# Kernel optimization log

Measured on AMD Instinct MI355X. Metric: run time of the kernel, lower is better.

Reference implementation:

```python
import jax, jax.numpy as jnp
import numpy as np

B, L, DM = 4, 2048, 1024  # batch, seq len (== l_max, global kernel), d_model; head_dim = 1


def setup_inputs() -> dict:
    key = jax.random.key(0)
    ks = jax.random.split(key, 13)
    n = lambda k, shape, s=1.0: jax.random.normal(k, shape, dtype=jnp.float32) * s
    W_SCALE = 0.02   # keeps activations well-conditioned through the chained convs
    K_SCALE = 0.02
    return {
        "u": n(ks[0], (B, L, DM)),
        "Wq": n(ks[1], (DM, DM), W_SCALE), "bq": n(ks[2], (DM,), W_SCALE),
        "Wk": n(ks[3], (DM, DM), W_SCALE), "bk": n(ks[4], (DM,), W_SCALE),
        "Wv": n(ks[5], (DM, DM), W_SCALE), "bv": n(ks[6], (DM,), W_SCALE),
        "k_kernel": n(ks[7], (DM, L), K_SCALE),
        "k_D": n(ks[8], (DM,)),
        "ssm_kernel": n(ks[9], (DM, L), K_SCALE),
        "D": n(ks[10], (DM,)),
        "Wo": n(ks[11], (DM, DM), W_SCALE), "bo": n(ks[12], (DM,), W_SCALE),
    }


def reference(u, Wq, bq, Wk, bk, Wv, bv, k_kernel, k_D, ssm_kernel, D, Wo, bo):
    # u: (B, L, H) with H = d_model (head_dim = 1)
    Lseq = u.shape[1]
    fft_size = 2 * Lseq  # zero-pad to 2L for linear (causal) convolution

    # q/k/v projections -> (B, H, L)
    q = jnp.einsum('blh,dh->bdl', u, Wq) + bq[None, :, None]
    k = jnp.einsum('blh,dh->bdl', u, Wk) + bk[None, :, None]
    v = jnp.einsum('blh,dh->bdl', u, Wv) + bv[None, :, None]

    # shift conv on k: k <- k_kernel * k (causal FFT conv) + k_D * k
    k_kernel_f = jnp.fft.rfft(k_kernel, n=fft_size)           # (H, F)
    k_f = jnp.fft.rfft(k, n=fft_size)                          # (B, H, F)
    shift_k = jnp.fft.irfft(k_kernel_f[None] * k_f, n=fft_size)[..., :Lseq]
    k = shift_k + k_D[None, :, None] * k

    # head_dim == 1: kv outer product collapses to elementwise gate
    kv = k * v                                                 # (B, H, L)

    # ssm conv on kv (torch's 1/fft_size + norm='forward' irfft == standard irfft)
    kv_f = jnp.fft.rfft(kv, n=fft_size)                        # (B, H, F)
    ssm_kernel_f = jnp.fft.rfft(ssm_kernel, n=fft_size)        # (H, F)
    y = jnp.fft.irfft(kv_f * ssm_kernel_f[None], n=fft_size)[..., :Lseq]
    y = y + kv * D[None, :, None]                              # D skip

    # q gating, then output projection
    y = y * q                                                  # (B, H, L)
    y = jnp.swapaxes(y, 1, 2)                                  # (B, L, H)
    return jnp.einsum('blh,oh->blo', y, Wo) + bo
```

## Files before the change

kernel.cpp:

```cpp
#include <hip/hip_runtime.h>
#include <hip/hip_bf16.h>
#include <stdint.h>

#define DM   1024
#define LSEQ 2048
#define NB   4

typedef __attribute__((ext_vector_type(8))) short  short8;
typedef __attribute__((ext_vector_type(4))) float  floatx4;

__device__ __forceinline__ ushort f2b(float x) {
    union { float f; uint32_t u; } v; v.f = x;
    uint32_t b = v.u + 0x7FFF + ((v.u >> 16) & 1);
    return (ushort)(b >> 16);
}
__device__ __forceinline__ float b2f(ushort x) {
    union { uint32_t u; float f; } v; v.u = ((uint32_t)x) << 16;
    return v.f;
}

__global__ __launch_bounds__(256) void cvt_all_kernel(const float* __restrict__ u,
                                                      const float* __restrict__ Wq,
                                                      const float* __restrict__ Wk,
                                                      const float* __restrict__ Wv,
                                                      const float* __restrict__ Wo,
                                                      ushort* __restrict__ U16,
                                                      ushort* __restrict__ Wcat) {
    const int nu  = NB * LSEQ * DM / 8;
    const int per = DM * DM / 8;
    int i = blockIdx.x * 256 + threadIdx.x;
    const float* src; ushort* dst; int j;
    if (i < nu) { src = u; dst = U16; j = i; }
    else {
        int k = i - nu;
        int r = k / per;
        src = (r == 0) ? Wq : (r == 1) ? Wk : (r == 2) ? Wv : Wo;
        dst = Wcat + (size_t)r * (DM * DM);
        j = k - r * per;
    }
    const float4* p = (const float4*)src + (size_t)j * 2;
    float4 a = p[0], b = p[1];
    union { ushort us[8]; uint4 v; } o;
    o.us[0] = f2b(a.x); o.us[1] = f2b(a.y); o.us[2] = f2b(a.z); o.us[3] = f2b(a.w);
    o.us[4] = f2b(b.x); o.us[5] = f2b(b.y); o.us[6] = f2b(b.z); o.us[7] = f2b(b.w);
    *(uint4*)(dst + (size_t)j * 8) = o.v;
}

template <int MODE, int BN>
__global__ __launch_bounds__(512, 2) void gemm_v2(const ushort* __restrict__ Aw,
                                                  const ushort* __restrict__ Bw,
                                                  const float* __restrict__ b0,
                                                  const float* __restrict__ b1,
                                                  const float* __restrict__ b2,
                                                  void* __restrict__ C0v,
                                                  void* __restrict__ C1v,
                                                  void* __restrict__ C2v,
                                                  int N, int nbx) {
    constexpr int K = 1024, BK = 64, NT = K / BK;
    constexpr int BM     = 128;
    constexpr int NJH    = BN / 128;
    constexpr int ASLOT  = BM * 128;
    constexpr int BSLOT  = BN * 128;
    constexpr int BOFF   = 2 * ASLOT;
    __shared__ char lds[BOFF + 2 * BSLOT];

    const int tid   = threadIdx.x;
    const int wave  = tid >> 6;
    const int lane  = tid & 63;
    const int qlane = lane & 15;
    const int qk    = lane >> 4;
    const int z7    = qlane & 7;
    const int wm    = wave >> 2;
    const int wn    = wave & 3;

    int flat = blockIdx.y * nbx + blockIdx.x;
    int nwg  = nbx * gridDim.y;
    int swz  = (flat & 7) * (nwg >> 3) + (flat >> 3);
    const int tn = (swz % nbx) * BN;
    const int tm = (swz / nbx) * BM;

    const int srcChunkOff = ((lane & 7) ^ (lane >> 3)) * 8;
    const int srcRow      = lane >> 3;

#define STAGE_A(TT)                                                                           \
    {                                                                                         \
        const int trow = tm + wave * 16 + srcRow;                                             \
        char* dst = lds + ((TT) & 1) * ASLOT + wave * 2048;                                   \
        const int k0_ = (TT) * BK;                                                            \
        _Pragma("unroll")                                                                     \
        for (int j = 0; j < 2; ++j) {                                                         \
            const ushort* src = Aw + (size_t)(trow + j * 8) * K + k0_ + srcChunkOff;          \
            __builtin_amdgcn_global_load_lds(                                                 \
                (const __attribute__((address_space(1))) void*)src,                           \
                (__attribute__((address_space(3))) void*)(dst + j * 1024), 16, 0, 0);         \
        }                                                                                     \
    }
#define STAGE_B(TT, H)                                                                        \
    {                                                                                         \
        const int rbase = (H) * (BN / 2) + wave * (8 * NJH);                                  \
        const int trow  = tn + rbase + srcRow;                                                \
        char* dst = lds + BOFF + ((TT) & 1) * BSLOT + rbase * 128;                            \
        const int k0_ = (TT) * BK;                                                            \
        _Pragma("unroll")                                                                     \
        for (int j = 0; j < NJH; ++j) {                                                       \
            const ushort* src = Bw + (size_t)(trow + j * 8) * K + k0_ + srcChunkOff;          \
            __builtin_amdgcn_global_load_lds(                                                 \
                (const __attribute__((address_space(1))) void*)src,                           \
                (__attribute__((address_space(3))) void*)(dst + j * 1024), 16, 0, 0);         \
        }                                                                                     \
    }

    short8 afA[4][2], afB[4][2], bf0[NJH][2], bf1[NJH][2];
    floatx4 acc[2][4][NJH] = {};

#define LDA(TT, AF)                                                                           \
    {                                                                                         \
        const char* Ab = lds + ((TT) & 1) * ASLOT;                                            \
        _Pragma("unroll")                                                                     \
        for (int i = 0; i < 4; ++i) {                                                         \
            int lr = wm * 64 + i * 16 + qlane;                                                \
            _Pragma("unroll")                                                                 \
            for (int ks = 0; ks < 2; ++ks)                                                    \
                AF[i][ks] = *(const short8*)(Ab + lr * 128 + (((ks * 4 + qk) ^ z7) << 4));    \
        }                                                                                     \
    }
#define LDB(TT, NH, BF)                                                                       \
    {                                                                                         \
        const char* Bb = lds + BOFF + ((TT) & 1) * BSLOT;                                     \
        _Pragma("unroll")                                                                     \
        for (int j = 0; j < NJH; ++j) {                                                       \
            int lr = wn * (BN / 4) + (NH) * (NJH * 16) + j * 16 + qlane;                      \
            _Pragma("unroll")                                                                 \
            for (int ks = 0; ks < 2; ++ks)                                                    \
                BF[j][ks] = *(const short8*)(Bb + lr * 128 + (((ks * 4 + qk) ^ z7) << 4));    \
        }                                                                                     \
    }
#define MFMAQ(NH, AF, BF)                                                                     \
    __builtin_amdgcn_s_setprio(1);                                                           \
    _Pragma("unroll")                                                                         \
    for (int ks = 0; ks < 2; ++ks)                                                            \
        _Pragma("unroll")                                                                     \
        for (int i = 0; i < 4; ++i)                                                           \
            _Pragma("unroll")                                                                 \
            for (int j = 0; j < NJH; ++j)                                                     \
                acc[NH][i][j] = __builtin_amdgcn_mfma_f32_16x16x32_bf16(                      \
                    AF[i][ks], BF[j][ks], acc[NH][i][j], 0, 0, 0);                            \
    __builtin_amdgcn_s_setprio(0);
#define BARX  __builtin_amdgcn_s_barrier(); __builtin_amdgcn_sched_barrier(0)
#define VM_STEADY                                                                             \
    do { if constexpr (BN == 384) asm volatile("s_waitcnt vmcnt(8)" ::: "memory");            \
         else                     asm volatile("s_waitcnt vmcnt(6)" ::: "memory"); } while (0)

    STAGE_A(0); STAGE_B(0, 0); STAGE_B(0, 1);
    STAGE_A(1); STAGE_B(1, 0); STAGE_B(1, 1);
    VM_STEADY;
    BARX;
    LDA(0, afA); LDB(0, 0, bf0);
    asm volatile("s_waitcnt lgkmcnt(0)" ::: "memory");
    __builtin_amdgcn_sched_barrier(0);
    BARX;

#define TILE(T, AFc, AFn)                                                                     \
    {                                                                                         \
        LDB(T, 1, bf1);                                                                       \
        MFMAQ(0, AFc, bf0);                                                                   \
        BARX;                                                                                 \
        if ((T) + 2 < NT) { STAGE_A((T) + 2); STAGE_B((T) + 2, 0); STAGE_B((T) + 2, 1); }     \
        MFMAQ(1, AFc, bf1);                                                                   \
        if ((T) + 2 < NT)      { VM_STEADY; }                                                 \
        else if ((T) + 1 < NT) { asm volatile("s_waitcnt vmcnt(0)" ::: "memory"); }           \
        BARX;                                                                                 \
        if ((T) + 1 < NT) { LDA((T) + 1, AFn); LDB((T) + 1, 0, bf0); }                        \
    }

    for (int t = 0; t < NT; t += 2) {
        TILE(t,     afA, afB);
        TILE(t + 1, afB, afA);
    }
#undef TILE
#undef STAGE_A
#undef STAGE_B
#undef LDA
#undef LDB
#undef MFMAQ
#undef BARX
#undef VM_STEADY

#pragma unroll
    for (int nh = 0; nh < 2; ++nh)
#pragma unroll
    for (int i = 0; i < 4; ++i)
#pragma unroll
    for (int j = 0; j < NJH; ++j) {
        int n  = tn + wn * (BN / 4) + nh * (NJH * 16) + j * 16 + qlane;
        int m0 = tm + wm * 64 + i * 16 + qk * 4;
        if (MODE == 0) {
            int proj = n >> 10, dd = n & (DM - 1);
            const float* bb = (proj == 0) ? b0 : (proj == 1) ? b1 : b2;
            ushort* Cb      = (ushort*)((proj == 0) ? C0v : (proj == 1) ? C1v : C2v);
            float bv = bb[dd];
            int b = m0 >> 11, l = m0 & (LSEQ - 1);
            ushort4 val;
            val.x = f2b(acc[nh][i][j][0] + bv);
            val.y = f2b(acc[nh][i][j][1] + bv);
            val.z = f2b(acc[nh][i][j][2] + bv);
            val.w = f2b(acc[nh][i][j][3] + bv);
            *(ushort4*)(Cb + ((size_t)b * DM + dd) * LSEQ + l) = val;
        } else {
            float* C0 = (float*)C0v;
            float bv = b0[n];
#pragma unroll
            for (int r = 0; r < 4; ++r)
                C0[(size_t)(m0 + r) * N + n] = acc[nh][i][j][r] + bv;
        }
    }
}

#define KSTR 2096
#define XSTR 2248

__global__ __launch_bounds__(256, 4) void conv_fused_kernel(const ushort* __restrict__ x,
                                                            const float* __restrict__ ker1,
                                                            const float* __restrict__ scale1,
                                                            const ushort* __restrict__ gate1,
                                                            const float* __restrict__ ker2,
                                                            const float* __restrict__ scale2,
                                                            const ushort* __restrict__ gate2,
                                                            ushort* __restrict__ out) {
    __shared__ ushort krev1[KSTR];
    __shared__ ushort krev2[KSTR];
    __shared__ ushort xs[4 * XSTR];
    const int d    = blockIdx.x;
    const int tid  = threadIdx.x;
    const int wave = tid >> 6;
    const int lane = tid & 63;

    {
        const ushort* src = x + ((size_t)wave * DM + d) * LSEQ + lane * 8;
        char* dst = (char*)xs + wave * (XSTR * 2) + 256;
#pragma unroll
        for (int c = 0; c < 4; ++c)
            __builtin_amdgcn_global_load_lds((const __attribute__((address_space(1))) void*)(src + c * 512),
                                             (__attribute__((address_space(3))) void*)(dst + c * 1024),
                                             16, 0, 0);
    }
    {
        int e0 = tid * 8;
        const float* k1p = ker1 + (size_t)d * LSEQ + e0;
        const float* k2p = ker2 + (size_t)d * LSEQ + e0;
        float4 a1 = *(const float4*)(k1p),     b1 = *(const float4*)(k1p + 4);
        float4 a2 = *(const float4*)(k2p),     b2 = *(const float4*)(k2p + 4);
        ushort4 o;
        o.x = f2b(a1.w); o.y = f2b(a1.z); o.z = f2b(a1.y); o.w = f2b(a1.x);
        *(ushort4*)(krev1 + (2060 - e0)) = o;
        o.x = f2b(b1.w); o.y = f2b(b1.z); o.z = f2b(b1.y); o.w = f2b(b1.x);
        *(ushort4*)(krev1 + (2056 - e0)) = o;
        o.x = f2b(a2.w); o.y = f2b(a2.z); o.z = f2b(a2.y); o.w = f2b(a2.x);
        *(ushort4*)(krev2 + (2060 - e0)) = o;
        o.x = f2b(b2.w); o.y = f2b(b2.z); o.z = f2b(b2.y); o.w = f2b(b2.x);
        *(ushort4*)(krev2 + (2056 - e0)) = o;
        uint4 z = {0, 0, 0, 0};
        if (tid < 2) {
            *(uint4*)((char*)krev1 + tid * 16) = z;
            *(uint4*)((char*)krev2 + tid * 16) = z;
        }
        if (tid >= 2 && tid < 6) {
            *(uint4*)((char*)krev1 + 4128 + (tid - 2) * 16) = z;
            *(uint4*)((char*)krev2 + 4128 + (tid - 2) * 16) = z;
        }
        if (tid >= 64 && tid < 128) {
            int b = (tid - 64) >> 4, c = (tid - 64) & 15;
            *(uint4*)((char*)xs + b * (XSTR * 2) + c * 16) = z;
        }
        if (tid >= 128 && tid < 144) {
            int b = (tid - 128) >> 2, c = (tid - 128) & 3;
            *(uint4*)((char*)xs + b * (XSTR * 2) + 4352 + c * 16) = z;
        }
    }
    __syncthreads();

    const int qn = lane & 15;
    const int qk = lane >> 4;

    int g[4] = {wave, 7 - wave, 8 + wave, 15 - wave};
    const int smax_all = 128 * (15 - wave) + 128;

    const int lbase = (qn & 3) * XSTR + 128 + 16 * (qn >> 2) + 8 * qk;

#define CSTEP(KR, ACC, SS, FP)                                                               \
    {                                                                                        \
        int b_el = 2063 - qn + 8 * qk - (SS);                                                \
        int A0 = b_el & ~3;                                                                  \
        uint2 w0 = *(const uint2*)((KR) + A0);                                               \
        uint2 w1 = *(const uint2*)((KR) + A0 + 4);                                           \
        uint2 w2 = *(const uint2*)((KR) + A0 + 8);                                           \
        int qsel = (b_el >> 1) & 1;                                                          \
        uint sh  = (uint)(b_el & 1) * 16u;                                                   \
        uint e0 = qsel ? w0.y : w0.x;                                                        \
        uint e1 = qsel ? w1.x : w0.y;                                                        \
        uint e2 = qsel ? w1.y : w1.x;                                                        \
        uint e3 = qsel ? w2.x : w1.y;                                                        \
        uint e4 = qsel ? w2.y : w2.x;                                                        \
        union { uint u[4]; short8 v; } Af;                                                   \
        Af.u[0] = __builtin_amdgcn_alignbit(e1, e0, sh);                                     \
        Af.u[1] = __builtin_amdgcn_alignbit(e2, e1, sh);                                     \
        Af.u[2] = __builtin_amdgcn_alignbit(e3, e2, sh);                                     \
        Af.u[3] = __builtin_amdgcn_alignbit(e4, e3, sh);                                     \
        _Pragma("unroll")                                                                    \
        for (int gi = 0; gi < 4; ++gi) {                                                     \
            if ((SS) <= 128 * g[gi] + 128) {                                                 \
                short8 fN = *(const short8*)(xs + lbase + 128 * g[gi] - (SS));               \
                ACC[gi][0] = __builtin_amdgcn_mfma_f32_16x16x32_bf16(Af.v, fN, ACC[gi][0], 0, 0, 0); \
                ACC[gi][1] = __builtin_amdgcn_mfma_f32_16x16x32_bf16(Af.v, FP[gi], ACC[gi][1], 0, 0, 0); \
                FP[gi] = fN;                                                                 \
            }                                                                                \
        }                                                                                    \
    }

    {
        floatx4 acc[4][2] = {};
        short8 fE[4], fO[4];
#pragma unroll
        for (int gi = 0; gi < 4; ++gi) {
            fE[gi] = *(const short8*)(xs + lbase + 128 * g[gi] + 64);
            fO[gi] = *(const short8*)(xs + lbase + 128 * g[gi] + 32);
        }
        for (int s = 0; s <= smax_all; s += 64) {
            CSTEP(krev1, acc, s, fE);
            if (s + 32 <= smax_all) CSTEP(krev1, acc, s + 32, fO);
        }

        __syncthreads();
        const float sc = scale1[d];
#pragma unroll
        for (int gi = 0; gi < 4; ++gi) {
#pragma unroll
            for (int m = 0; m < 2; ++m) {
                int p  = 8 * g[gi] + 4 * m + (qn >> 2);
                int b  = qn & 3;
                int l0 = 16 * p + 4 * qk;
                size_t off = ((size_t)b * DM + d) * LSEQ + l0;
                ushort4 xv = *(const ushort4*)(xs + b * XSTR + 128 + l0);
                ushort4 gv = *(const ushort4*)(gate1 + off);
                ushort4 ov;
                ov.x = f2b((acc[gi][m][0] + sc * b2f(xv.x)) * b2f(gv.x));
                ov.y = f2b((acc[gi][m][1] + sc * b2f(xv.y)) * b2f(gv.y));
                ov.z = f2b((acc[gi][m][2] + sc * b2f(xv.z)) * b2f(gv.z));
                ov.w = f2b((acc[gi][m][3] + sc * b2f(xv.w)) * b2f(gv.w));
                *(ushort4*)(xs + b * XSTR + 128 + l0) = ov;
            }
        }
        __syncthreads();
    }

    {
        floatx4 acc[4][2] = {};
        short8 fE[4], fO[4];
#pragma unroll
        for (int gi = 0; gi < 4; ++gi) {
            fE[gi] = *(const short8*)(xs + lbase + 128 * g[gi] + 64);
            fO[gi] = *(const short8*)(xs + lbase + 128 * g[gi] + 32);
        }
        for (int s = 0; s <= smax_all; s += 64) {
            CSTEP(krev2, acc, s, fE);
            if (s + 32 <= smax_all) CSTEP(krev2, acc, s + 32, fO);
        }

        const float sc = scale2[d];
#pragma unroll
        for (int gi = 0; gi < 4; ++gi) {
#pragma unroll
            for (int m = 0; m < 2; ++m) {
                int p  = 8 * g[gi] + 4 * m + (qn >> 2);
                int b  = qn & 3;
                int l0 = 16 * p + 4 * qk;
                size_t off = ((size_t)b * DM + d) * LSEQ + l0;
                ushort4 xv = *(const ushort4*)(xs + b * XSTR + 128 + l0);
                ushort4 gv = *(const ushort4*)(gate2 + off);
                ushort4 ov;
                ov.x = f2b((acc[gi][m][0] + sc * b2f(xv.x)) * b2f(gv.x));
                ov.y = f2b((acc[gi][m][1] + sc * b2f(xv.y)) * b2f(gv.y));
                ov.z = f2b((acc[gi][m][2] + sc * b2f(xv.z)) * b2f(gv.z));
                ov.w = f2b((acc[gi][m][3] + sc * b2f(xv.w)) * b2f(gv.w));
                *(ushort4*)(out + off) = ov;
            }
        }
    }
#undef CSTEP
}

__global__ __launch_bounds__(256) void transpose_bf16(const ushort* __restrict__ in,
                                                      ushort* __restrict__ out) {
    __shared__ ushort t[32][36];
    const int l0 = blockIdx.x * 32;
    const int d0 = blockIdx.y * 32;
    const int b  = blockIdx.z;
    const int q  = threadIdx.x & 7;
    const int r  = threadIdx.x >> 3;
    *(ushort4*)(&t[r][q * 4]) = *(const ushort4*)(in + ((size_t)b * DM + d0 + r) * LSEQ + l0 + q * 4);
    __syncthreads();
    ushort4 o;
    o.x = t[q * 4 + 0][r]; o.y = t[q * 4 + 1][r]; o.z = t[q * 4 + 2][r]; o.w = t[q * 4 + 3][r];
    *(ushort4*)(out + ((size_t)b * LSEQ + l0 + r) * DM + d0 + q * 4) = o;
}

extern "C" void kernel_launch(void* const* d_in, const int* in_sizes, int n_in,
                              void* d_out, int out_size, void* d_ws, size_t ws_size,
                              hipStream_t stream) {
    const float* u        = (const float*)d_in[0];
    const float* Wq       = (const float*)d_in[1];
    const float* bq       = (const float*)d_in[2];
    const float* Wk       = (const float*)d_in[3];
    const float* bk       = (const float*)d_in[4];
    const float* Wv       = (const float*)d_in[5];
    const float* bv       = (const float*)d_in[6];
    const float* k_kernel = (const float*)d_in[7];
    const float* k_D      = (const float*)d_in[8];
    const float* ssm_ker  = (const float*)d_in[9];
    const float* Dv       = (const float*)d_in[10];
    const float* Wo       = (const float*)d_in[11];
    const float* bo       = (const float*)d_in[12];
    float* outp = (float*)d_out;

    char* ws = (char*)d_ws;
    ushort* Q    = (ushort*)(ws);
    ushort* KV   = (ushort*)(ws + (16ull << 20));
    ushort* V    = (ushort*)(ws + (32ull << 20));
    ushort* U16  = (ushort*)(ws + (48ull << 20));
    ushort* YT   = (ushort*)(ws + (64ull << 20));
    ushort* Wcat = (ushort*)(ws + (80ull << 20));

    const int nu = NB * LSEQ * DM / 8, nw = 4 * DM * DM / 8;
    cvt_all_kernel<<<(nu + nw) / 256, 256, 0, stream>>>(u, Wq, Wk, Wv, Wo, U16, Wcat);

    dim3 g1(3 * DM / 384, NB * LSEQ / 128);
    gemm_v2<0, 384><<<g1, 512, 0, stream>>>(U16, Wcat, bq, bk, bv, Q, KV, V,
                                            3 * DM, 3 * DM / 384);

    conv_fused_kernel<<<DM, 256, 0, stream>>>(KV, k_kernel, k_D, V, ssm_ker, Dv, Q, KV);

    dim3 g2(LSEQ / 32, DM / 32, NB);
    transpose_bf16<<<g2, 256, 0, stream>>>(KV, YT);

    dim3 g3(DM / 256, NB * LSEQ / 128);
    gemm_v2<1, 256><<<g3, 512, 0, stream>>>(YT, Wcat + 3 * DM * DM, bo, bo, bo,
                                            outp, outp, outp, DM, DM / 256);
}
```

Measured before the change: 158.6 us.

## Replace QKV projection GEMM with 4-wave 256x192 tile kernel

Adds a new GEMM kernel for the fused QKV projection. It uses 256-thread blocks of four waves, each computing a 128x96 sub-tile, with a 256x192 block tile and double-buffered direct global-to-LDS loads. Prefetch runs two K-steps ahead, and wavefront priority is raised around the MFMA bursts. This replaces the previous 512-thread 128x384 tiling. The aim is higher arithmetic intensity per wave and better overlap of loads with MFMA. The trade-off is much higher register pressure from 48 accumulator tiles per wave, which may limit occupancy to one block per SIMD group, and a different grid shape (16x32 blocks).

```diff
diff --git a/kernel.cpp b/kernel.cpp
--- a/kernel.cpp
+++ b/kernel.cpp
@@ -44,6 +44,137 @@
     o.us[0] = f2b(a.x); o.us[1] = f2b(a.y); o.us[2] = f2b(a.z); o.us[3] = f2b(a.w);
     o.us[4] = f2b(b.x); o.us[5] = f2b(b.y); o.us[6] = f2b(b.z); o.us[7] = f2b(b.w);
     *(uint4*)(dst + (size_t)j * 8) = o.v;
+}
+
+__global__ __launch_bounds__(256, 1) void gemm_v3(const ushort* __restrict__ Aw,
+                                                  const ushort* __restrict__ Bw,
+                                                  const float* __restrict__ b0,
+                                                  const float* __restrict__ b1,
+                                                  const float* __restrict__ b2,
+                                                  ushort* __restrict__ C0,
+                                                  ushort* __restrict__ C1,
+                                                  ushort* __restrict__ C2,
+                                                  int N, int nbx) {
+    constexpr int K = 1024, BK = 64, NT = K / BK;
+    constexpr int BM = 256, BN = 192;
+    constexpr int ASLOT = BM * 128;
+    constexpr int BSLOT = BN * 128;
+    constexpr int BOFF  = 2 * ASLOT;
+    __shared__ char lds[BOFF + 2 * BSLOT];
+
+    const int tid   = threadIdx.x;
+    const int wave  = tid >> 6;
+    const int lane  = tid & 63;
+    const int qlane = lane & 15;
+    const int qk    = lane >> 4;
+    const int z7    = qlane & 7;
+    const int wm    = wave >> 1;
+    const int wn    = wave & 1;
+
+    int flat = blockIdx.y * nbx + blockIdx.x;
+    int nwg  = nbx * gridDim.y;
+    int swz  = (flat & 7) * (nwg >> 3) + (flat >> 3);
+    const int tn = (swz % nbx) * BN;
+    const int tm = (swz / nbx) * BM;
+
+    const int srcChunkOff = ((lane & 7) ^ (lane >> 3)) * 8;
+    const int srcRow      = lane >> 3;
+
+#define STAGE3(TT)                                                                            \
+    {                                                                                         \
+        const int k0_ = (TT) * BK;                                                            \
+        char* dstA = lds + ((TT) & 1) * ASLOT + wave * 8192;                                  \
+        const int ra = tm + wave * 64 + srcRow;                                               \
+        _Pragma("unroll")                                                                     \
+        for (int jj = 0; jj < 8; ++jj) {                                                      \
+            const ushort* src = Aw + (size_t)(ra + jj * 8) * K + k0_ + srcChunkOff;           \
+            __builtin_amdgcn_global_load_lds(                                                 \
+                (const __attribute__((address_space(1))) void*)src,                           \
+                (__attribute__((address_space(3))) void*)(dstA + jj * 1024), 16, 0, 0);       \
+        }                                                                                     \
+        char* dstB = lds + BOFF + ((TT) & 1) * BSLOT + wave * 6144;                           \
+        const int rb = tn + wave * 48 + srcRow;                                               \
+        _Pragma("unroll")                                                                     \
+        for (int jj = 0; jj < 6; ++jj) {                                                      \
+            const ushort* src = Bw + (size_t)(rb + jj * 8) * K + k0_ + srcChunkOff;           \
+            __builtin_amdgcn_global_load_lds(                                                 \
+                (const __attribute__((address_space(1))) void*)src,                           \
+                (__attribute__((address_space(3))) void*)(dstB + jj * 1024), 16, 0, 0);       \
+        }                                                                                     \
+    }
+
+    short8 af0[8], af1[8], bf0[6], bf1[6];
+    floatx4 acc[8][6] = {};
+
+#define LD3A(TT, KS, AF)                                                                      \
+    {                                                                                         \
+        const char* Ab = lds + ((TT) & 1) * ASLOT;                                            \
+        _Pragma("unroll")                                                                     \
+        for (int i = 0; i < 8; ++i)                                                           \
+            AF[i] = *(const short8*)(Ab + (wm * 128 + i * 16 + qlane) * 128 +                 \
+                                     ((((KS) * 4 + qk) ^ z7) << 4));                          \
+    }
+#define LD3B(TT, KS, BF)                                                                      \
+    {                                                                                         \
+        const char* Bb = lds + BOFF + ((TT) & 1) * BSLOT;                                     \
+        _Pragma("unroll")                                                                     \
+        for (int j = 0; j < 6; ++j)                                                           \
+            BF[j] = *(const short8*)(Bb + (wn * 96 + j * 16 + qlane) * 128 +                  \
+                                     ((((KS) * 4 + qk) ^ z7) << 4));                          \
+    }
+#define MFMAQ3(AF, BF)                                                                        \
+    __builtin_amdgcn_s_setprio(1);                                                           \
+    _Pragma("unroll")                                                                         \
+    for (int i = 0; i < 8; ++i)                                                               \
+        _Pragma("unroll")                                                                     \
+        for (int j = 0; j < 6; ++j)                                                           \
+            acc[i][j] = __builtin_amdgcn_mfma_f32_16x16x32_bf16(AF[i], BF[j], acc[i][j], 0, 0, 0); \
+    __builtin_amdgcn_s_setprio(0);
+#define BARX  __builtin_amdgcn_s_barrier(); __builtin_amdgcn_sched_barrier(0)
+
+    STAGE3(0); STAGE3(1);
+    asm volatile("s_waitcnt vmcnt(14)" ::: "memory");
+    BARX;
+    LD3A(0, 0, af0); LD3B(0, 0, bf0);
+    asm volatile("s_waitcnt lgkmcnt(0)" ::: "memory");
+    __builtin_amdgcn_sched_barrier(0);
+    BARX;
+
+    for (int t = 0; t < NT; ++t) {
+        LD3A(t, 1, af1); LD3B(t, 1, bf1);
+        MFMAQ3(af0, bf0);
+        BARX;
+        if (t + 2 < NT) STAGE3(t + 2);
+        MFMAQ3(af1, bf1);
+        if (t + 2 < NT)      { asm volatile("s_waitcnt vmcnt(14)" ::: "memory"); }
+        else if (t + 1 < NT) { asm volatile("s_waitcnt vmcnt(0)"  ::: "memory"); }
+        BARX;
+        if (t + 1 < NT) { LD3A(t + 1, 0, af0); LD3B(t + 1, 0, bf0); }
+    }
+#undef STAGE3
+#undef LD3A
+#undef LD3B
+#undef MFMAQ3
+#undef BARX
+
+#pragma unroll
+    for (int i = 0; i < 8; ++i)
+#pragma unroll
+    for (int j = 0; j < 6; ++j) {
+        int n  = tn + wn * 96 + j * 16 + qlane;
+        int m0 = tm + wm * 128 + i * 16 + qk * 4;
+        int proj = n >> 10, dd = n & (DM - 1);
+        const float* bb = (proj == 0) ? b0 : (proj == 1) ? b1 : b2;
+        ushort* Cb      = (proj == 0) ? C0 : (proj == 1) ? C1 : C2;
+        float bv = bb[dd];
+        int b = m0 >> 11, l = m0 & (LSEQ - 1);
+        ushort4 val;
+        val.x = f2b(acc[i][j][0] + bv);
+        val.y = f2b(acc[i][j][1] + bv);
+        val.z = f2b(acc[i][j][2] + bv);
+        val.w = f2b(acc[i][j][3] + bv);
+        *(ushort4*)(Cb + ((size_t)b * DM + dd) * LSEQ + l) = val;
+    }
 }
 
 template <int MODE, int BN>
@@ -433,9 +564,9 @@
     const int nu = NB * LSEQ * DM / 8, nw = 4 * DM * DM / 8;
     cvt_all_kernel<<<(nu + nw) / 256, 256, 0, stream>>>(u, Wq, Wk, Wv, Wo, U16, Wcat);
 
-    dim3 g1(3 * DM / 384, NB * LSEQ / 128);
-    gemm_v2<0, 384><<<g1, 512, 0, stream>>>(U16, Wcat, bq, bk, bv, Q, KV, V,
-                                            3 * DM, 3 * DM / 384);
+    dim3 g1(3 * DM / 192, NB * LSEQ / 256);
+    gemm_v3<<<g1, 256, 0, stream>>>(U16, Wcat, bq, bk, bv, Q, KV, V,
+                                    3 * DM, 3 * DM / 192);
 
     conv_fused_kernel<<<DM, 256, 0, stream>>>(KV, k_kernel, k_D, V, ssm_ker, Dv, Q, KV);
 
```

Result: slower. 165.9 us (+4.6%).
